# Performance work log

Measured on AMD Instinct MI355X. Metric: run time of the kernel, lower is better.

Reference implementation:

```python
import jax, jax.numpy as jnp
import numpy as np

MICRO_BATCHES = 2
TOP_K = 2
D = 512
E = 8  # num_experts (world_size=1 -> all local)
B, S = 8, 8192


def setup_inputs() -> dict:
    key = jax.random.key(0)
    ks = jax.random.split(key, 12)
    s = 0.02
    return {
        "x": jax.random.normal(ks[0], (B, S, D), dtype=jnp.float32),
        "ln_g": jnp.ones((D,), jnp.float32),
        "ln_b": jnp.zeros((D,), jnp.float32),
        "attn_w": jax.random.normal(ks[1], (D, D), jnp.float32) * s,
        "attn_b": jnp.zeros((D,), jnp.float32),
        "gate_w": jax.random.normal(ks[2], (E, D), jnp.float32) * s,
        "fc1_w": jax.random.normal(ks[3], (E, 4 * D, D), jnp.float32) * s,
        "fc1_b": jnp.zeros((E, 4 * D), jnp.float32),
        "fc2_w": jax.random.normal(ks[4], (E, D, 4 * D), jnp.float32) * s,
        "fc2_b": jnp.zeros((E, D), jnp.float32),
        "next_w": jax.random.normal(ks[5], (D, D), jnp.float32) * s,
        "next_b": jnp.zeros((D,), jnp.float32),
    }


def reference(x, ln_g, ln_b, attn_w, attn_b, gate_w, fc1_w, fc1_b, fc2_w, fc2_b, next_w, next_b):
    b, s, d = x.shape
    xf = x.reshape(b * s, d)
    # attn_norm -> attn linear + residual
    mu = jnp.mean(xf, axis=-1, keepdims=True)
    var = jnp.var(xf, axis=-1, keepdims=True)
    normed = (xf - mu) / jnp.sqrt(var + 1e-5) * ln_g + ln_b
    x_attn = normed @ attn_w.T + attn_b + xf
    # gating: logits + top-k (computed in the original but unused for the output path)
    logits = x_attn @ gate_w.T
    _scores, _indices = jax.lax.top_k(logits, TOP_K)
    # dispatch (identity all_to_all at world_size=1): tokens split positionally
    # into MICRO_BATCHES micro-batches, each chunked into E equal expert slices
    e = fc1_w.shape[0]
    t = (b * s) // (MICRO_BATCHES * e)  # tokens per expert per micro-batch
    tok = x_attn.reshape(MICRO_BATCHES, e, t, d)  # [m,e,t,d]
    h = jnp.einsum("meti,ehi->meth", tok, fc1_w) + fc1_b[None, :, None, :]
    h = jax.nn.gelu(h, approximate=False)  # torch nn.GELU default = erf
    y = jnp.einsum("meth,edh->metd", h, fc2_w) + fc2_b[None, :, None, :]
    # combine (identity) + next_layer_ops (Linear -> GELU), order preserved by cat
    yf = y.reshape(b * s, d)
    out = jax.nn.gelu(yf @ next_w.T + next_b, approximate=False)
    return out.reshape(b, s, d)
```

## Files before the change

kernel.cpp:

```cpp
#include <hip/hip_runtime.h>
#include <math.h>

typedef __bf16 bf16x8 __attribute__((ext_vector_type(8)));
typedef float f32x4 __attribute__((ext_vector_type(4)));
typedef unsigned short us4v __attribute__((ext_vector_type(4)));
typedef unsigned short us8v __attribute__((ext_vector_type(8)));

#define NTOK 65536
#define DMODEL 512

__device__ __forceinline__ unsigned short f2bf(float f) {
  unsigned int u = __float_as_uint(f);
  u += 0x7fffu + ((u >> 16) & 1u);
  return (unsigned short)(u >> 16);
}

__device__ __forceinline__ float gelu_fast(float x) {
  float x3 = x * x * x;
  float u = __expf(1.5957691216057308f * (x + 0.044715f * x3));
  return x * __fdividef(u, u + 1.0f);
}

__device__ __forceinline__ void async16(const void* g, void* l) {
  __builtin_amdgcn_global_load_lds((const __attribute__((address_space(1))) void*)g,
                                   (__attribute__((address_space(3))) void*)l,
                                   16, 0, 0);
}

__global__ __launch_bounds__(256) void cvt_bf16_kernel(const float4* __restrict__ in,
                                                       us4v* __restrict__ out, int n4) {
  int i = blockIdx.x * 256 + threadIdx.x;
  if (i < n4) {
    float4 v = in[i];
    us4v o;
    o.x = f2bf(v.x); o.y = f2bf(v.y); o.z = f2bf(v.z); o.w = f2bf(v.w);
    out[i] = o;
  }
}

__global__ __launch_bounds__(256) void ln_kernel(const float* __restrict__ x,
                                                 const float* __restrict__ g,
                                                 const float* __restrict__ b,
                                                 unsigned short* __restrict__ out) {
  const int w = threadIdx.x >> 6;
  const int lane = threadIdx.x & 63;
  const size_t row = (size_t)blockIdx.x * 4 + w;
  const float4* xv = (const float4*)(x + row * DMODEL);
  float4 v0 = xv[lane * 2];
  float4 v1 = xv[lane * 2 + 1];
  float s  = v0.x + v0.y + v0.z + v0.w + v1.x + v1.y + v1.z + v1.w;
  float ss = v0.x*v0.x + v0.y*v0.y + v0.z*v0.z + v0.w*v0.w
           + v1.x*v1.x + v1.y*v1.y + v1.z*v1.z + v1.w*v1.w;
#pragma unroll
  for (int m = 1; m < 64; m <<= 1) {
    s  += __shfl_xor(s, m, 64);
    ss += __shfl_xor(ss, m, 64);
  }
  const float mean = s * (1.0f / DMODEL);
  const float var  = ss * (1.0f / DMODEL) - mean * mean;
  const float rstd = rsqrtf(var + 1e-5f);
  const int c = lane * 8;
  const float4* gv = (const float4*)(g + c);
  const float4* bv = (const float4*)(b + c);
  float4 g0 = gv[0], g1 = gv[1], bb0 = bv[0], bb1 = bv[1];
  us8v o;
  o[0] = f2bf((v0.x - mean) * rstd * g0.x + bb0.x);
  o[1] = f2bf((v0.y - mean) * rstd * g0.y + bb0.y);
  o[2] = f2bf((v0.z - mean) * rstd * g0.z + bb0.z);
  o[3] = f2bf((v0.w - mean) * rstd * g0.w + bb0.w);
  o[4] = f2bf((v1.x - mean) * rstd * g1.x + bb1.x);
  o[5] = f2bf((v1.y - mean) * rstd * g1.y + bb1.y);
  o[6] = f2bf((v1.z - mean) * rstd * g1.z + bb1.z);
  o[7] = f2bf((v1.w - mean) * rstd * g1.w + bb1.w);
  *(us8v*)(out + row * DMODEL + c) = o;
}

#define MFMA_Q(mh, nh)                                                           \
  {                                                                              \
    _Pragma("unroll") for (int s = 0; s < 2; ++s)                                \
        _Pragma("unroll") for (int mi = 0; mi < 4; ++mi)                         \
            _Pragma("unroll") for (int ni = 0; ni < 2; ++ni)                     \
                acc[(mh) * 4 + mi][(nh) * 2 + ni] =                              \
        __builtin_amdgcn_mfma_f32_16x16x32_bf16(af[s][(mh) * 4 + mi],            \
                                                bfr[s][(nh) * 2 + ni],           \
                                                acc[(mh) * 4 + mi][(nh) * 2 + ni],\
                                                0, 0, 0);                        \
  }

template <int EPI, bool EXPERT, typename OutT, int K>
__global__ __launch_bounds__(512, 2) void gemm8p(
    const unsigned short* __restrict__ A, const unsigned short* __restrict__ B,
    const float* __restrict__ bias, const float* __restrict__ resid,
    OutT* __restrict__ C, int N) {
  __shared__ alignas(16) unsigned short lds[2][2][16384];
  const int tid = threadIdx.x;
  const int w = tid >> 6;
  const int lane = tid & 63;
  const int wm = w >> 2, wn = w & 3;
  const int quad = lane >> 4, lm = lane & 15;

  const int ncol = N >> 8;
  const int perx = gridDim.x >> 3;
  const int xcd = blockIdx.x & 7;
  const int wk = xcd * perx + (blockIdx.x >> 3);
  const int band_rows = (K == 2048) ? 2 : (ncol >= 8 ? 4 : 8);
  const int bb = band_rows * ncol;
  const int band = wk / bb;
  const int rem = wk - band * bb;
  const int ct = rem / band_rows;
  const int rib = rem - ct * band_rows;
  const size_t row0 = (size_t)(band * band_rows + rib) * 256;
  const int col0 = ct * 256;

  const unsigned short* Bp = B;
  const float* biasp = bias;
  if (EXPERT) {
    const int e = (int)((row0 >> 12) & 7);
    Bp += (size_t)e * (size_t)N * (size_t)K;
    biasp += (size_t)e * (size_t)N;
  }

  const int r0 = w * 32 + (lane >> 3);
  const int kg0 = (lane & 7) ^ (lane >> 3);
  const unsigned short* gA = A + (row0 + (size_t)r0) * (size_t)K + kg0 * 8;
  const unsigned short* gB = Bp + ((size_t)col0 + (size_t)r0) * (size_t)K + kg0 * 8;

  auto stageA = [&](int buf, const unsigned short* p) {
    unsigned short* l = &lds[buf][0][(w * 4) * 512];
    async16(p, l);
    async16(p + 8 * K, l + 512);
    async16(p + 16 * K, l + 1024);
    async16(p + 24 * K, l + 1536);
  };
  auto stageB = [&](int buf, const unsigned short* p) {
    unsigned short* l = &lds[buf][1][(w * 4) * 512];
    async16(p, l);
    async16(p + 8 * K, l + 512);
    async16(p + 16 * K, l + 1024);
    async16(p + 24 * K, l + 1536);
  };

  f32x4 acc[8][4] = {};
  const int NT = K / 64;

  stageA(0, gA);
  stageB(0, gB);
  stageA(1, gA + 64);
  stageB(1, gB + 64);
  gA += 128;
  gB += 128;
  asm volatile("s_waitcnt vmcnt(8)" ::: "memory");
  __builtin_amdgcn_s_barrier();

  for (int t = 0; t < NT; ++t) {
    const unsigned short* tA = &lds[t & 1][0][0];
    const unsigned short* tB = &lds[t & 1][1][0];
    const bool st = (t + 2 < NT);
    bf16x8 af[2][8], bfr[2][4];

#pragma unroll
    for (int s = 0; s < 2; ++s) {
#pragma unroll
      for (int mi = 0; mi < 4; ++mi) {
        const int r = wm * 128 + mi * 16 + lm;
        af[s][mi] = *(const bf16x8*)&tA[(r * 8 + ((s * 4 + quad) ^ (r & 7))) * 8];
      }
#pragma unroll
      for (int ni = 0; ni < 2; ++ni) {
        const int c = wn * 64 + ni * 16 + lm;
        bfr[s][ni] = *(const bf16x8*)&tB[(c * 8 + ((s * 4 + quad) ^ (c & 7))) * 8];
      }
    }
    __builtin_amdgcn_s_barrier();
    asm volatile("s_waitcnt lgkmcnt(0)" ::: "memory");
    __builtin_amdgcn_s_setprio(1);
    MFMA_Q(0, 0);
    __builtin_amdgcn_s_setprio(0);
    __builtin_amdgcn_s_barrier();

#pragma unroll
    for (int s = 0; s < 2; ++s) {
#pragma unroll
      for (int mi = 0; mi < 4; ++mi) {
        const int r = wm * 128 + (mi + 4) * 16 + lm;
        af[s][mi + 4] = *(const bf16x8*)&tA[(r * 8 + ((s * 4 + quad) ^ (r & 7))) * 8];
      }
#pragma unroll
      for (int ni = 0; ni < 2; ++ni) {
        const int c = wn * 64 + (ni + 2) * 16 + lm;
        bfr[s][ni + 2] = *(const bf16x8*)&tB[(c * 8 + ((s * 4 + quad) ^ (c & 7))) * 8];
      }
    }
    __builtin_amdgcn_s_barrier();
    asm volatile("s_waitcnt lgkmcnt(0)" ::: "memory");
    __builtin_amdgcn_s_setprio(1);
    MFMA_Q(0, 1);
    __builtin_amdgcn_s_setprio(0);
    __builtin_amdgcn_s_barrier();

    if (st) stageA(t & 1, gA);
    __builtin_amdgcn_s_barrier();
    __builtin_amdgcn_s_setprio(1);
    MFMA_Q(1, 0);
    __builtin_amdgcn_s_setprio(0);
    __builtin_amdgcn_s_barrier();

    if (st) {
      stageB(t & 1, gB);
      gA += 64;
      gB += 64;
    }
    __builtin_amdgcn_s_barrier();
    __builtin_amdgcn_s_setprio(1);
    MFMA_Q(1, 1);
    __builtin_amdgcn_s_setprio(0);

    if (t < NT - 2) {
      asm volatile("s_waitcnt vmcnt(8)" ::: "memory");
      __builtin_amdgcn_s_barrier();
    } else if (t == NT - 2) {
      asm volatile("s_waitcnt vmcnt(0)" ::: "memory");
      __builtin_amdgcn_s_barrier();
    }
  }

#pragma unroll
  for (int mi = 0; mi < 8; ++mi) {
#pragma unroll
    for (int ni = 0; ni < 4; ++ni) {
      const int col = col0 + wn * 64 + ni * 16 + lm;
      const float bv = biasp[col];
#pragma unroll
      for (int r = 0; r < 4; ++r) {
        const size_t grow = row0 + (size_t)(wm * 128 + mi * 16 + quad * 4 + r);
        float v = acc[mi][ni][r] + bv;
        if constexpr (EPI == 0) v += resid[grow * (size_t)N + col];
        if constexpr (EPI == 1) v = gelu_fast(v);
        if constexpr (sizeof(OutT) == 4) {
          C[grow * (size_t)N + col] = v;
        } else {
          C[grow * (size_t)N + col] = (OutT)f2bf(v);
        }
      }
    }
  }
}

extern "C" void kernel_launch(void* const* d_in, const int* in_sizes, int n_in,
                              void* d_out, int out_size, void* d_ws, size_t ws_size,
                              hipStream_t stream) {
  const float* x      = (const float*)d_in[0];
  const float* ln_g   = (const float*)d_in[1];
  const float* ln_b   = (const float*)d_in[2];
  const float* attn_w = (const float*)d_in[3];
  const float* attn_b = (const float*)d_in[4];
  const float* fc1_w  = (const float*)d_in[6];
  const float* fc1_b  = (const float*)d_in[7];
  const float* fc2_w  = (const float*)d_in[8];
  const float* fc2_b  = (const float*)d_in[9];
  const float* next_w = (const float*)d_in[10];
  const float* next_b = (const float*)d_in[11];

  char* ws = (char*)d_ws;
  const size_t MB = 1024ull * 1024ull;
  unsigned short* wN    = (unsigned short*)(ws);
  unsigned short* wXat  = (unsigned short*)(ws + 64 * MB);
  unsigned short* wH    = (unsigned short*)(ws + 128 * MB);
  unsigned short* attnbf = (unsigned short*)(ws + 384 * MB);
  unsigned short* fc1bf  = (unsigned short*)(ws + 385 * MB);
  unsigned short* fc2bf  = (unsigned short*)(ws + 401 * MB);
  unsigned short* nextbf = (unsigned short*)(ws + 417 * MB);

  {
    int n4;
    n4 = (512 * 512) / 4;
    cvt_bf16_kernel<<<dim3((n4 + 255) / 256), dim3(256), 0, stream>>>((const float4*)attn_w, (us4v*)attnbf, n4);
    n4 = (8 * 2048 * 512) / 4;
    cvt_bf16_kernel<<<dim3((n4 + 255) / 256), dim3(256), 0, stream>>>((const float4*)fc1_w, (us4v*)fc1bf, n4);
    n4 = (8 * 512 * 2048) / 4;
    cvt_bf16_kernel<<<dim3((n4 + 255) / 256), dim3(256), 0, stream>>>((const float4*)fc2_w, (us4v*)fc2bf, n4);
    n4 = (512 * 512) / 4;
    cvt_bf16_kernel<<<dim3((n4 + 255) / 256), dim3(256), 0, stream>>>((const float4*)next_w, (us4v*)nextbf, n4);
  }

  ln_kernel<<<dim3(NTOK / 4), dim3(256), 0, stream>>>(x, ln_g, ln_b, wN);

  gemm8p<0, false, unsigned short, 512><<<dim3((NTOK / 256) * 2), dim3(512), 0, stream>>>(
      wN, attnbf, attn_b, x, wXat, 512);

  gemm8p<1, true, unsigned short, 512><<<dim3((NTOK / 256) * 8), dim3(512), 0, stream>>>(
      wXat, fc1bf, fc1_b, nullptr, wH, 2048);

  gemm8p<2, true, unsigned short, 2048><<<dim3((NTOK / 256) * 2), dim3(512), 0, stream>>>(
      wH, fc2bf, fc2_b, nullptr, wN, 512);

  gemm8p<1, false, float, 512><<<dim3((NTOK / 256) * 2), dim3(512), 0, stream>>>(
      wN, nextbf, next_b, nullptr, (float*)d_out, 512);
}
```

Baseline: 803.3 us.

## Restructure GEMM main loop to prefetch next tile fragments into registers

Replaces the four-phase ping-pong loop, which had barriers between each quarter of the MFMA work, with a register double-buffered schedule. The first half of the A/B fragments for the next K-tile is read from LDS at the end of each iteration, the second half at the start, and all four MFMA quadrants then run back-to-back. Global-to-LDS staging of both A and B is issued together after a single barrier. This is meant to cut barrier count and hide LDS read latency behind MFMAs, at the cost of more live vector registers under 512-thread, 2-block launch bounds, which risks spills or lower occupancy.

```diff
diff --git a/kernel.cpp b/kernel.cpp
--- a/kernel.cpp
+++ b/kernel.cpp
@@ -75,20 +75,47 @@
   *(us8v*)(out + row * DMODEL + c) = o;
 }
 
-#define MFMA_Q(mh, nh)                                                           \
-  {                                                                              \
-    _Pragma("unroll") for (int s = 0; s < 2; ++s)                                \
-        _Pragma("unroll") for (int mi = 0; mi < 4; ++mi)                         \
-            _Pragma("unroll") for (int ni = 0; ni < 2; ++ni)                     \
-                acc[(mh) * 4 + mi][(nh) * 2 + ni] =                              \
-        __builtin_amdgcn_mfma_f32_16x16x32_bf16(af[s][(mh) * 4 + mi],            \
-                                                bfr[s][(nh) * 2 + ni],           \
-                                                acc[(mh) * 4 + mi][(nh) * 2 + ni],\
-                                                0, 0, 0);                        \
-  }
+template <int HALF>
+__device__ __forceinline__ void rd_a(bf16x8* d, const unsigned short* tA,
+                                     int wm, int lm, int quad) {
+#pragma unroll
+  for (int s = 0; s < 2; ++s)
+#pragma unroll
+    for (int mi = 0; mi < 4; ++mi) {
+      const int r = wm * 128 + (HALF * 4 + mi) * 16 + lm;
+      d[s * 4 + mi] = *(const bf16x8*)&tA[(r * 8 + ((s * 4 + quad) ^ (r & 7))) * 8];
+    }
+}
+
+template <int HALF>
+__device__ __forceinline__ void rd_b(bf16x8* d, const unsigned short* tB,
+                                     int wn, int lm, int quad) {
+#pragma unroll
+  for (int s = 0; s < 2; ++s)
+#pragma unroll
+    for (int ni = 0; ni < 2; ++ni) {
+      const int c = wn * 64 + (HALF * 2 + ni) * 16 + lm;
+      d[s * 2 + ni] = *(const bf16x8*)&tB[(c * 8 + ((s * 4 + quad) ^ (c & 7))) * 8];
+    }
+}
+
+template <int MO, int NO>
+__device__ __forceinline__ void quad_mfma(f32x4 (&acc)[8][4], const bf16x8* a,
+                                          const bf16x8* b) {
+  __builtin_amdgcn_s_setprio(1);
+#pragma unroll
+  for (int s = 0; s < 2; ++s)
+#pragma unroll
+    for (int mi = 0; mi < 4; ++mi)
+#pragma unroll
+      for (int ni = 0; ni < 2; ++ni)
+        acc[MO + mi][NO + ni] = __builtin_amdgcn_mfma_f32_16x16x32_bf16(
+            a[s * 4 + mi], b[s * 2 + ni], acc[MO + mi][NO + ni], 0, 0, 0);
+  __builtin_amdgcn_s_setprio(0);
+}
 
 template <int EPI, bool EXPERT, typename OutT, int K>
-__global__ __launch_bounds__(512, 2) void gemm8p(
+__global__ __launch_bounds__(512, 2) void gemmP(
     const unsigned short* __restrict__ A, const unsigned short* __restrict__ B,
     const float* __restrict__ bias, const float* __restrict__ resid,
     OutT* __restrict__ C, int N) {
@@ -141,6 +168,7 @@
   };
 
   f32x4 acc[8][4] = {};
+  bf16x8 a0[8], b0[4], a1[8], b1[4];
   const int NT = K / 64;
 
   stageA(0, gA);
@@ -151,77 +179,34 @@
   gB += 128;
   asm volatile("s_waitcnt vmcnt(8)" ::: "memory");
   __builtin_amdgcn_s_barrier();
+  rd_a<0>(a0, &lds[0][0][0], wm, lm, quad);
+  rd_b<0>(b0, &lds[0][1][0], wn, lm, quad);
+  __builtin_amdgcn_sched_barrier(0);
 
   for (int t = 0; t < NT; ++t) {
-    const unsigned short* tA = &lds[t & 1][0][0];
-    const unsigned short* tB = &lds[t & 1][1][0];
-    const bool st = (t + 2 < NT);
-    bf16x8 af[2][8], bfr[2][4];
-
-#pragma unroll
-    for (int s = 0; s < 2; ++s) {
-#pragma unroll
-      for (int mi = 0; mi < 4; ++mi) {
-        const int r = wm * 128 + mi * 16 + lm;
-        af[s][mi] = *(const bf16x8*)&tA[(r * 8 + ((s * 4 + quad) ^ (r & 7))) * 8];
-      }
-#pragma unroll
-      for (int ni = 0; ni < 2; ++ni) {
-        const int c = wn * 64 + ni * 16 + lm;
-        bfr[s][ni] = *(const bf16x8*)&tB[(c * 8 + ((s * 4 + quad) ^ (c & 7))) * 8];
-      }
-    }
+    const int cur = t & 1;
+    rd_b<1>(b1, &lds[cur][1][0], wn, lm, quad);
+    rd_a<1>(a1, &lds[cur][0][0], wm, lm, quad);
+    __builtin_amdgcn_sched_barrier(0);
+    quad_mfma<0, 0>(acc, a0, b0);
+    quad_mfma<0, 2>(acc, a0, b1);
+    quad_mfma<4, 0>(acc, a1, b0);
+    quad_mfma<4, 2>(acc, a1, b1);
+    if (t == NT - 1) break;
     __builtin_amdgcn_s_barrier();
-    asm volatile("s_waitcnt lgkmcnt(0)" ::: "memory");
-    __builtin_amdgcn_s_setprio(1);
-    MFMA_Q(0, 0);
-    __builtin_amdgcn_s_setprio(0);
-    __builtin_amdgcn_s_barrier();
-
-#pragma unroll
-    for (int s = 0; s < 2; ++s) {
-#pragma unroll
-      for (int mi = 0; mi < 4; ++mi) {
-        const int r = wm * 128 + (mi + 4) * 16 + lm;
-        af[s][mi + 4] = *(const bf16x8*)&tA[(r * 8 + ((s * 4 + quad) ^ (r & 7))) * 8];
-      }
-#pragma unroll
-      for (int ni = 0; ni < 2; ++ni) {
-        const int c = wn * 64 + (ni + 2) * 16 + lm;
-        bfr[s][ni + 2] = *(const bf16x8*)&tB[(c * 8 + ((s * 4 + quad) ^ (c & 7))) * 8];
-      }
-    }
-    __builtin_amdgcn_s_barrier();
-    asm volatile("s_waitcnt lgkmcnt(0)" ::: "memory");
-    __builtin_amdgcn_s_setprio(1);
-    MFMA_Q(0, 1);
-    __builtin_amdgcn_s_setprio(0);
-    __builtin_amdgcn_s_barrier();
-
-    if (st) stageA(t & 1, gA);
-    __builtin_amdgcn_s_barrier();
-    __builtin_amdgcn_s_setprio(1);
-    MFMA_Q(1, 0);
-    __builtin_amdgcn_s_setprio(0);
-    __builtin_amdgcn_s_barrier();
-
-    if (st) {
-      stageB(t & 1, gB);
+    if (t + 2 < NT) {
+      stageA(cur, gA);
+      stageB(cur, gB);
       gA += 64;
       gB += 64;
+      asm volatile("s_waitcnt vmcnt(8)" ::: "memory");
+    } else {
+      asm volatile("s_waitcnt vmcnt(0)" ::: "memory");
     }
     __builtin_amdgcn_s_barrier();
-    __builtin_amdgcn_s_setprio(1);
-    MFMA_Q(1, 1);
-    __builtin_amdgcn_s_setprio(0);
-
-    if (t < NT - 2) {
-      asm volatile("s_waitcnt vmcnt(8)" ::: "memory");
-      __builtin_amdgcn_s_barrier();
-    } else if (t == NT - 2) {
-      asm volatile("s_waitcnt vmcnt(0)" ::: "memory");
-      __builtin_amdgcn_s_barrier();
-    }
+    rd_a<0>(a0, &lds[cur ^ 1][0][0], wm, lm, quad);
+    rd_b<0>(b0, &lds[cur ^ 1][1][0], wn, lm, quad);
+    __builtin_amdgcn_sched_barrier(0);
   }
 
 #pragma unroll
@@ -285,15 +270,15 @@
 
   ln_kernel<<<dim3(NTOK / 4), dim3(256), 0, stream>>>(x, ln_g, ln_b, wN);
 
-  gemm8p<0, false, unsigned short, 512><<<dim3((NTOK / 256) * 2), dim3(512), 0, stream>>>(
+  gemmP<0, false, unsigned short, 512><<<dim3((NTOK / 256) * 2), dim3(512), 0, stream>>>(
       wN, attnbf, attn_b, x, wXat, 512);
 
-  gemm8p<1, true, unsigned short, 512><<<dim3((NTOK / 256) * 8), dim3(512), 0, stream>>>(
+  gemmP<1, true, unsigned short, 512><<<dim3((NTOK / 256) * 8), dim3(512), 0, stream>>>(
       wXat, fc1bf, fc1_b, nullptr, wH, 2048);
 
-  gemm8p<2, true, unsigned short, 2048><<<dim3((NTOK / 256) * 2), dim3(512), 0, stream>>>(
+  gemmP<2, true, unsigned short, 2048><<<dim3((NTOK / 256) * 2), dim3(512), 0, stream>>>(
       wH, fc2bf, fc2_b, nullptr, wN, 512);
 
-  gemm8p<1, false, float, 512><<<dim3((NTOK / 256) * 2), dim3(512), 0, stream>>>(
+  gemmP<1, false, float, 512><<<dim3((NTOK / 256) * 2), dim3(512), 0, stream>>>(
       wN, nextbf, next_b, nullptr, (float*)d_out, 512);
 }
```

Result: slower. 877.7 us (+9.3%).
